# Optimization experiments

Measured on AMD Instinct MI355X. Metric: run time of the kernel, lower is better.

Reference implementation:

```python
import jax, jax.numpy as jnp
import numpy as np
import math

D_MODEL = 1024
N_HEADS = 16
D_HEAD = D_MODEL // N_HEADS
DECAY_MAX = 0.99  # buggy torch init: only the LAST head's decay rate survives the loop
LN_EPS = 1e-5


def setup_inputs() -> dict:
    key = jax.random.key(0)
    ks = jax.random.split(key, 12)
    B, S = 2, 2048
    x = jax.random.normal(ks[0], (B, S, D_MODEL), dtype=jnp.float32)
    def w(k):
        return jax.random.normal(k, (D_MODEL, D_MODEL), dtype=jnp.float32) * 0.02
    return {
        "x": x,
        "Wq": w(ks[1]), "bq": jnp.zeros((D_MODEL,), jnp.float32),
        "Wk": w(ks[2]), "bk": jnp.zeros((D_MODEL,), jnp.float32),
        "Wv": w(ks[3]), "bv": jnp.zeros((D_MODEL,), jnp.float32),
        "Wg": w(ks[4]), "bg": jnp.zeros((D_MODEL,), jnp.float32),
        "Wo": w(ks[5]), "bo": jnp.zeros((D_MODEL,), jnp.float32),
        "gamma": jnp.ones((D_MODEL,), jnp.float32),
        "beta": jnp.zeros((D_MODEL,), jnp.float32),
    }


def _decay_mask(S):
    # faithful to torch buffer: decay_matrix[i,j] = DECAY_MAX**(i-j) for j<=i else 0
    i = jnp.arange(S, dtype=jnp.float32)[:, None]
    j = jnp.arange(S, dtype=jnp.float32)[None, :]
    diff = i - j
    return jnp.where(diff >= 0, jnp.power(jnp.float32(DECAY_MAX), diff), 0.0)  # [S,S]


def reference(x, Wq, bq, Wk, bk, Wv, bv, Wg, bg, Wo, bo, gamma, beta):
    B, S, D = x.shape
    H, DH = N_HEADS, D_HEAD
    # projections -> [B,H,S,DH]
    Q = (x @ Wq + bq).reshape(B, S, H, DH).transpose(0, 2, 1, 3)
    K = (x @ Wk + bk).reshape(B, S, H, DH).transpose(0, 2, 1, 3)
    V = (x @ Wv + bv).reshape(B, S, H, DH).transpose(0, 2, 1, 3)
    scores = jnp.einsum('bhsd,bhtd->bhst', Q, K) / math.sqrt(DH)  # [B,H,S,S]
    mask = _decay_mask(S)  # [S,S], broadcast over B,H (head-independent per torch bug)
    retained = jnp.einsum('bhst,bhtd->bhsd', scores * mask, V)
    retained = retained.transpose(0, 2, 1, 3).reshape(B, S, D)
    # LayerNorm over last dim
    mu = jnp.mean(retained, axis=-1, keepdims=True)
    var = jnp.var(retained, axis=-1, keepdims=True)
    normed = (retained - mu) * jax.lax.rsqrt(var + LN_EPS) * gamma + beta
    G = jax.nn.sigmoid(x @ Wg + bg)
    return (normed * G) @ Wo + bo  # dropout = identity (eval)
```

## Files before the change

kernel.cpp:

```cpp
#include <hip/hip_runtime.h>

typedef __attribute__((ext_vector_type(4))) float f32x4;
typedef __attribute__((ext_vector_type(8))) short bf16x8;
typedef unsigned short USHORT;

static __device__ __forceinline__ float bf2f(USHORT u) {
    return __uint_as_float(((unsigned)u) << 16);
}
static __device__ __forceinline__ USHORT f2bf(float f) {
    unsigned u = __float_as_uint(f);
    unsigned r = u + 0x7FFF + ((u >> 16) & 1);
    return (USHORT)(r >> 16);
}

#define GLDS16(gp, lp) __builtin_amdgcn_global_load_lds(                      \
    (const __attribute__((address_space(1))) unsigned int*)(gp),              \
    (__attribute__((address_space(3))) unsigned int*)(lp), 16, 0, 0)

#define FULL_BARRIER() asm volatile("s_waitcnt vmcnt(0) lgkmcnt(0)\ns_barrier" ::: "memory")

#define D64 0.52559648f
#define L2D (-0.014499569695115089f)

struct PrepArgs { const float* src[5]; USHORT* dst[5]; const float* x; USHORT* xb; };

__global__ __launch_bounds__(256) void k_prep(PrepArgs pa) {
    const int z = blockIdx.z;
    const int tid = threadIdx.x;
    __shared__ USHORT t[64][65];
    if (z < 5) {
        const float* __restrict__ W  = pa.src[z];
        USHORT* __restrict__      WT = pa.dst[z];
        const int k0 = blockIdx.y * 64, n0 = blockIdx.x * 64;
#pragma unroll
        for (int s = 0; s < 4; s++) {
            int slot = tid + s * 256;
            int row = slot >> 4, c4 = (slot & 15) * 4;
            float4 vv = *(const float4*)&W[(size_t)(k0 + row) * 1024 + n0 + c4];
            t[row][c4 + 0] = f2bf(vv.x);
            t[row][c4 + 1] = f2bf(vv.y);
            t[row][c4 + 2] = f2bf(vv.z);
            t[row][c4 + 3] = f2bf(vv.w);
        }
        __syncthreads();
#pragma unroll
        for (int s = 0; s < 2; s++) {
            int slot = tid + s * 256;
            int n = slot >> 3, c8 = (slot & 7) * 8;
            USHORT tmp[8];
#pragma unroll
            for (int u = 0; u < 8; u++) tmp[u] = t[c8 + u][n];
            *(int4*)&WT[(size_t)(n0 + n) * 1024 + k0 + c8] = *(int4*)tmp;
        }
    } else {
        const int bi = blockIdx.y * 16 + blockIdx.x;
        const float* xs = pa.x + (size_t)bi * 16384;
        USHORT* xd = pa.xb + (size_t)bi * 16384;
#pragma unroll
        for (int u = 0; u < 16; u++) {
            int idx = u * 1024 + tid * 4;
            float4 v = *(const float4*)&xs[idx];
            *(ushort4*)&xd[idx] = make_ushort4(f2bf(v.x), f2bf(v.y), f2bf(v.z), f2bf(v.w));
        }
    }
}

struct GArgs {
    const USHORT* A;
    const USHORT* W[4];
    const float*  bias[4];
    void*         dst[4];
    USHORT*       dstv;
    float         scale[4];
    int           mode[4];
};


__global__ __launch_bounds__(256, 2) void k_gemm(GArgs ga) {
    const int z = blockIdx.z;
    const USHORT* __restrict__ A  = ga.A;
    const USHORT* __restrict__ BT = ga.W[z];
    __shared__ USHORT As[2][128 * 32];
    __shared__ USHORT Bs[2][128 * 32];
    const int tid = threadIdx.x;
    const int m0 = blockIdx.y * 128, n0 = blockIdx.x * 128;
    const int w = tid >> 6, l = tid & 63, lr = l & 15, q = l >> 4;
    const int wr = w >> 1, wc = w & 1;
    const int srow = tid >> 2, sco = (tid & 3) * 8;
    const int scol = (((tid & 3) ^ ((tid >> 3) & 3)) << 3);
    const int kread = ((q ^ ((lr >> 1) & 3)) << 3);
    f32x4 acc[4][4] = {};
    GLDS16(&A [(size_t)(m0 + srow)      * 1024 + scol], &As[0][srow * 32 + sco]);
    GLDS16(&A [(size_t)(m0 + srow + 64) * 1024 + scol], &As[0][(srow + 64) * 32 + sco]);
    GLDS16(&BT[(size_t)(n0 + srow)      * 1024 + scol], &Bs[0][srow * 32 + sco]);
    GLDS16(&BT[(size_t)(n0 + srow + 64) * 1024 + scol], &Bs[0][(srow + 64) * 32 + sco]);
    for (int kt = 0; kt < 32; kt++) {
        const int cur = kt & 1;
        FULL_BARRIER();
        if (kt + 1 < 32) {
            const int k1 = (kt + 1) * 32;
            const int nxt = 1 - cur;
            GLDS16(&A [(size_t)(m0 + srow)      * 1024 + k1 + scol], &As[nxt][srow * 32 + sco]);
            GLDS16(&A [(size_t)(m0 + srow + 64) * 1024 + k1 + scol], &As[nxt][(srow + 64) * 32 + sco]);
            GLDS16(&BT[(size_t)(n0 + srow)      * 1024 + k1 + scol], &Bs[nxt][srow * 32 + sco]);
            GLDS16(&BT[(size_t)(n0 + srow + 64) * 1024 + k1 + scol], &Bs[nxt][(srow + 64) * 32 + sco]);
        }
        bf16x8 af[4], bfr[4];
#pragma unroll
        for (int mi = 0; mi < 4; mi++)
            af[mi] = *(const bf16x8*)&As[cur][(wr * 64 + mi * 16 + lr) * 32 + kread];
#pragma unroll
        for (int ni = 0; ni < 4; ni++)
            bfr[ni] = *(const bf16x8*)&Bs[cur][(wc * 64 + ni * 16 + lr) * 32 + kread];
#pragma unroll
        for (int mi = 0; mi < 4; mi++)
#pragma unroll
            for (int ni = 0; ni < 4; ni++)
                acc[mi][ni] = __builtin_amdgcn_mfma_f32_16x16x32_bf16(
                    af[mi], bfr[ni], acc[mi][ni], 0, 0, 0);
    }
    const float scale = ga.scale[z];
    const int mode = ga.mode[z];
    const float* __restrict__ bias = ga.bias[z];
#pragma unroll
    for (int ni = 0; ni < 4; ni++) {
        int col = n0 + wc * 64 + ni * 16 + lr;
        float bv = bias[col];
#pragma unroll
        for (int mi = 0; mi < 4; mi++) {
            int r0 = m0 + wr * 64 + mi * 16 + q * 4;
            float vr[4];
#pragma unroll
            for (int r = 0; r < 4; r++) {
                float v = acc[mi][ni][r] + bv;
                if (mode == 1) v = 1.0f / (1.0f + __expf(-v));
                vr[r] = v * scale;
            }
            if (mode == 3) {
                float* df = (float*)ga.dst[z];
#pragma unroll
                for (int r = 0; r < 4; r++)
                    df[(size_t)(r0 + r) * 1024 + col] = vr[r];
            } else if (mode == 2) {
                int b = r0 >> 11, s = r0 & 2047;
                int h = col >> 6, d = col & 63;
                const float NP1 = 1.0101010101010102f;
                float c0 = exp2f(-L2D * (float)(s & 63));
                float c1 = c0 * NP1, c2 = c1 * NP1, c3 = c2 * NP1;
                *(ushort4*)&ga.dstv[(size_t)(((b * 16 + h) * 64) + d) * 2048 + s] =
                    make_ushort4(f2bf(vr[0] * c0), f2bf(vr[1] * c1),
                                 f2bf(vr[2] * c2), f2bf(vr[3] * c3));
            } else {
                USHORT* db = (USHORT*)ga.dst[z];
#pragma unroll
                for (int r = 0; r < 4; r++)
                    db[(size_t)(r0 + r) * 1024 + col] = f2bf(vr[r]);
            }
        }
    }
}

__global__ __launch_bounds__(256, 2) void k_gemm_out(const USHORT* __restrict__ A,
                                                     const USHORT* __restrict__ BT,
                                                     const float* __restrict__ bias,
                                                     float* __restrict__ C) {
    __shared__ USHORT As[2][64 * 32];
    __shared__ USHORT Bs[2][128 * 32];
    const int tid = threadIdx.x;
    const int m0 = blockIdx.y * 64, n0 = blockIdx.x * 128;
    const int w = tid >> 6, l = tid & 63, lr = l & 15, q = l >> 4;
    const int srow = tid >> 2, sco = (tid & 3) * 8;
    const int scol = (((tid & 3) ^ ((tid >> 3) & 3)) << 3);
    const int kread = ((q ^ ((lr >> 1) & 3)) << 3);
    f32x4 acc[4][2] = {};
    GLDS16(&A [(size_t)(m0 + srow)      * 1024 + scol], &As[0][srow * 32 + sco]);
    GLDS16(&BT[(size_t)(n0 + srow)      * 1024 + scol], &Bs[0][srow * 32 + sco]);
    GLDS16(&BT[(size_t)(n0 + srow + 64) * 1024 + scol], &Bs[0][(srow + 64) * 32 + sco]);
    for (int kt = 0; kt < 32; kt++) {
        const int cur = kt & 1;
        FULL_BARRIER();
        if (kt + 1 < 32) {
            const int k1 = (kt + 1) * 32;
            const int nxt = 1 - cur;
            GLDS16(&A [(size_t)(m0 + srow)      * 1024 + k1 + scol], &As[nxt][srow * 32 + sco]);
            GLDS16(&BT[(size_t)(n0 + srow)      * 1024 + k1 + scol], &Bs[nxt][srow * 32 + sco]);
            GLDS16(&BT[(size_t)(n0 + srow + 64) * 1024 + k1 + scol], &Bs[nxt][(srow + 64) * 32 + sco]);
        }
        bf16x8 af[4], bfr[2];
#pragma unroll
        for (int mi = 0; mi < 4; mi++)
            af[mi] = *(const bf16x8*)&As[cur][(mi * 16 + lr) * 32 + kread];
#pragma unroll
        for (int ni = 0; ni < 2; ni++)
            bfr[ni] = *(const bf16x8*)&Bs[cur][(w * 32 + ni * 16 + lr) * 32 + kread];
#pragma unroll
        for (int mi = 0; mi < 4; mi++)
#pragma unroll
            for (int ni = 0; ni < 2; ni++)
                acc[mi][ni] = __builtin_amdgcn_mfma_f32_16x16x32_bf16(
                    af[mi], bfr[ni], acc[mi][ni], 0, 0, 0);
    }
#pragma unroll
    for (int ni = 0; ni < 2; ni++) {
        const int col = n0 + w * 32 + ni * 16 + lr;
        const float bv = bias[col];
#pragma unroll
        for (int mi = 0; mi < 4; mi++) {
            const int r0 = m0 + mi * 16 + q * 4;
#pragma unroll
            for (int r = 0; r < 4; r++)
                C[(size_t)(r0 + r) * 1024 + col] = acc[mi][ni][r] + bv;
        }
    }
}

#define LDSA(buf, kh) (((buf) * 2 + (kh)) * 8192)
#define LDSB(buf, kh) (32768 + ((buf) * 2 + (kh)) * 8192)
#define BAR() asm volatile("s_barrier" ::: "memory")
#define VM8() asm volatile("s_waitcnt vmcnt(8)" ::: "memory")

#define STAGE_A(ks, kh, buf) do {                                             \
    const USHORT* s_ = aBase + (ks) * 64 + (kh) * 32;                         \
    GLDS16(s_,          &lds[LDSA(buf, kh) + ldsT]);                          \
    GLDS16(s_ + 131072, &lds[LDSA(buf, kh) + 4096 + ldsT]); } while (0)

#define STAGE_B(ks, kh, buf) do {                                             \
    const USHORT* s_ = bBase + (ks) * 64 + (kh) * 32;                         \
    GLDS16(s_,          &lds[LDSB(buf, kh) + ldsT]);                          \
    GLDS16(s_ + 131072, &lds[LDSB(buf, kh) + 4096 + ldsT]); } while (0)

#define PHASE256(buf, kh, mg, LOADB, STAGE_STMT, WAITSTMT) do {               \
    _Pragma("unroll")                                                         \
    for (int mi = 0; mi < 4; mi++)                                            \
        af[mi] = *(const bf16x8*)&lds[LDSA(buf, kh) + aoff + ((mg) * 4 + mi) * 512]; \
    if (LOADB) {                                                              \
        _Pragma("unroll")                                                     \
        for (int ni = 0; ni < 4; ni++)                                        \
            bfrag[ni] = *(const bf16x8*)&lds[LDSB(buf, kh) + boff + ni * 512];\
    }                                                                         \
    STAGE_STMT;                                                               \
    BAR();                                                                    \
    __builtin_amdgcn_s_setprio(1);                                            \
    _Pragma("unroll")                                                         \
    for (int mi = 0; mi < 4; mi++)                                            \
        _Pragma("unroll")                                                     \
        for (int ni = 0; ni < 4; ni++)                                        \
            acc[(mg) * 4 + mi][ni] = __builtin_amdgcn_mfma_f32_16x16x32_bf16( \
                af[mi], bfrag[ni], acc[(mg) * 4 + mi][ni], 0, 0, 0);          \
    __builtin_amdgcn_s_setprio(0);                                            \
    WAITSTMT;                                                                 \
    BAR();                                                                    \
} while (0)

__global__ __launch_bounds__(512, 2) void k_gemm256(GArgs ga) {
    extern __shared__ USHORT lds[];
    int bid = blockIdx.x + 4 * (blockIdx.y + 16 * blockIdx.z);
    bid = (bid & 7) * 32 + (bid >> 3);
    const int bz = bid >> 6;
    const int by = (bid >> 2) & 15;
    const int bx = bid & 3;
    const int z = bz;
    const USHORT* __restrict__ A  = ga.A;
    const USHORT* __restrict__ BT = ga.W[z];
    const int m0 = by * 256, n0 = bx * 256;
    const int tid = threadIdx.x;
    const int wid = tid >> 6, l = tid & 63, lr = l & 15, q = l >> 4;
    const int wr = wid >> 2, wc = wid & 3;
    const int srow = tid >> 2;
    const int scol = (((tid & 3) ^ ((tid >> 3) & 3)) << 3);
    const USHORT* aBase = A  + (size_t)(m0 + srow) * 1024 + scol;
    const USHORT* bBase = BT + (size_t)(n0 + srow) * 1024 + scol;
    const int ldsT = tid * 8;
    const int kread = ((q ^ ((lr >> 1) & 3)) << 3);
    const int aoff = (wr * 128 + lr) * 32 + kread;
    const int boff = (wc * 64 + lr) * 32 + kread;
    f32x4 acc[8][4] = {};
    bf16x8 af[4], bfrag[4];

    STAGE_A(0, 0, 0); STAGE_B(0, 0, 0);
    STAGE_A(0, 1, 0); STAGE_B(0, 1, 0);
    STAGE_A(1, 0, 1); STAGE_B(1, 0, 1);
    VM8();
    BAR();

    for (int kt = 0; kt < 16; kt += 2) {
        const int ks1 = kt + 1;
        const int ks2 = (kt + 2 < 16) ? kt + 2 : 15;
        const int ks3 = (kt + 2 < 16) ? kt + 2 : 15;
        const int ks4 = (kt + 3 < 16) ? kt + 3 : 15;
        PHASE256(0, 0, 0, 1, STAGE_A(ks1, 1, 1), (void)0);
        PHASE256(0, 0, 1, 0, STAGE_B(ks1, 1, 1), VM8());
        PHASE256(0, 1, 0, 1, STAGE_A(ks2, 0, 0), (void)0);
        PHASE256(0, 1, 1, 0, STAGE_B(ks2, 0, 0), VM8());
        PHASE256(1, 0, 0, 1, STAGE_A(ks3, 1, 0), (void)0);
        PHASE256(1, 0, 1, 0, STAGE_B(ks3, 1, 0), VM8());
        PHASE256(1, 1, 0, 1, STAGE_A(ks4, 0, 1), (void)0);
        PHASE256(1, 1, 1, 0, STAGE_B(ks4, 0, 1), VM8());
    }

    const float scale = ga.scale[z];
    const int mode = ga.mode[z];
    const float* __restrict__ bias = ga.bias[z];
#pragma unroll
    for (int ni = 0; ni < 4; ni++) {
        int col = n0 + wc * 64 + ni * 16 + lr;
        float bv = bias[col];
#pragma unroll
        for (int mi = 0; mi < 8; mi++) {
            int r0 = m0 + wr * 128 + mi * 16 + q * 4;
            float vr[4];
#pragma unroll
            for (int r = 0; r < 4; r++) {
                float v = acc[mi][ni][r] + bv;
                if (mode == 1) v = 1.0f / (1.0f + __expf(-v));
                vr[r] = v * scale;
            }
            if (mode == 3) {
                float* df = (float*)ga.dst[z];
#pragma unroll
                for (int r = 0; r < 4; r++)
                    df[(size_t)(r0 + r) * 1024 + col] = vr[r];
            } else if (mode == 2) {
                int b = r0 >> 11, s = r0 & 2047;
                int h = col >> 6, d = col & 63;
                const float NP1 = 1.0101010101010102f;
                float c0 = exp2f(-L2D * (float)(s & 63));
                float c1 = c0 * NP1, c2 = c1 * NP1, c3 = c2 * NP1;
                *(ushort4*)&ga.dstv[(size_t)(((b * 16 + h) * 64) + d) * 2048 + s] =
                    make_ushort4(f2bf(vr[0] * c0), f2bf(vr[1] * c1),
                                 f2bf(vr[2] * c2), f2bf(vr[3] * c3));
            } else {
                USHORT* db = (USHORT*)ga.dst[z];
#pragma unroll
                for (int r = 0; r < 4; r++)
                    db[(size_t)(r0 + r) * 1024 + col] = f2bf(vr[r]);
            }
        }
    }
}

__global__ __launch_bounds__(256) void k_attn_u(const USHORT* __restrict__ K,
                                                const USHORT* __restrict__ VT,
                                                float* __restrict__ U) {
    const int bh = blockIdx.x, c = blockIdx.y;
    const int b = bh >> 4, h = bh & 15;
    const int tid = threadIdx.x, w = tid >> 6, l = tid & 63, lr = l & 15, q = l >> 4;
    __shared__ USHORT KT[64 * 72];
    __shared__ USHORT Vs[64 * 72];
#pragma unroll
    for (int s = 0; s < 2; s++) {
        int slot = tid + s * 256;
        int row = slot >> 3, co = (slot & 7) * 8;
        USHORT kv[8];
        *(int4*)kv = *(const int4*)&K[(size_t)(b * 2048 + c * 64 + row) * 1024 + h * 64 + co];
#pragma unroll
        for (int u = 0; u < 8; u++) KT[(co + u) * 72 + row] = kv[u];
        *(int4*)&Vs[row * 72 + co] =
            *(const int4*)&VT[(size_t)(bh * 64 + row) * 2048 + c * 64 + co];
    }
    __syncthreads();
    f32x4 acc[4] = {};
    bf16x8 av[2];
#pragma unroll
    for (int kk = 0; kk < 2; kk++)
        av[kk] = *(const bf16x8*)&Vs[(w * 16 + lr) * 72 + kk * 32 + q * 8];
#pragma unroll
    for (int dkt = 0; dkt < 4; dkt++)
#pragma unroll
        for (int kk = 0; kk < 2; kk++) {
            bf16x8 bk = *(const bf16x8*)&KT[(dkt * 16 + lr) * 72 + kk * 32 + q * 8];
            acc[dkt] = __builtin_amdgcn_mfma_f32_16x16x32_bf16(av[kk], bk, acc[dkt], 0, 0, 0);
        }
    float* slot = U + (size_t)(bh * 32 + c) * 4096;
#pragma unroll
    for (int dkt = 0; dkt < 4; dkt++)
#pragma unroll
        for (int r = 0; r < 4; r++)
            slot[(w * 16 + q * 4 + r) * 64 + dkt * 16 + lr] = acc[dkt][r] * D64;
}

__global__ __launch_bounds__(256) void k_scan(float* __restrict__ U) {
    const int bh = blockIdx.x;
    const int idx4 = blockIdx.y * 256 + threadIdx.x;
    float* base = U + (size_t)bh * 32 * 4096 + idx4 * 4;
    float4 s = make_float4(0.f, 0.f, 0.f, 0.f);
    for (int c = 0; c < 32; c++) {
        float* p = base + (size_t)c * 4096;
        float4 v = *(const float4*)p;
        s.x = s.x * D64 + v.x;
        s.y = s.y * D64 + v.y;
        s.z = s.z * D64 + v.z;
        s.w = s.w * D64 + v.w;
        *(float4*)p = s;
    }
}

__global__ __launch_bounds__(256, 2) void k_apply(const USHORT* __restrict__ Q,
                                                  const USHORT* __restrict__ K,
                                                  const USHORT* __restrict__ VT,
                                                  const float* __restrict__ U,
                                                  USHORT* __restrict__ R,
                                                  float* __restrict__ stats) {
    const int bh = blockIdx.x, c = blockIdx.y;
    const int b = bh >> 4, h = bh & 15;
    const int i0 = c * 64;
    const int tid = threadIdx.x, w = tid >> 6, l = tid & 63, lr = l & 15, q = l >> 4;
    __shared__ USHORT Qs[64 * 72];
    __shared__ USHORT Ks[64 * 72];
    __shared__ USHORT Vs[64 * 72];
    __shared__ USHORT Ps[4][16 * 72];
    __shared__ unsigned Spk[4096];
#pragma unroll
    for (int s = 0; s < 2; s++) {
        int slot = tid + s * 256;
        int row = slot >> 3, c8 = (slot & 7) * 8;
        USHORT q8[8];
        *(int4*)q8 = *(const int4*)&Q[(size_t)(b * 2048 + i0 + row) * 1024 + h * 64 + c8];
        const float fr = exp2f(L2D * (float)row);
#pragma unroll
        for (int u = 0; u < 8; u++) q8[u] = f2bf(bf2f(q8[u]) * fr);
        *(int4*)&Qs[row * 72 + c8] = *(int4*)q8;
        *(int4*)&Ks[row * 72 + c8] =
            *(const int4*)&K[(size_t)(b * 2048 + i0 + row) * 1024 + h * 64 + c8];
        *(int4*)&Vs[row * 72 + c8] =
            *(const int4*)&VT[(size_t)(bh * 64 + row) * 2048 + i0 + c8];
    }
    if (c > 0) {
        const float* p = U + (size_t)(bh * 32 + (c - 1)) * 4096 + tid * 16;
        float sa[16];
#pragma unroll
        for (int u4 = 0; u4 < 4; u4++) {
            float4 uv = *(const float4*)(p + u4 * 4);
            sa[u4 * 4 + 0] = uv.x; sa[u4 * 4 + 1] = uv.y;
            sa[u4 * 4 + 2] = uv.z; sa[u4 * 4 + 3] = uv.w;
        }
#pragma unroll
        for (int u = 0; u < 16; u++) {
            USHORT hi = f2bf(sa[u]);
            float  lo = sa[u] - bf2f(hi);
            Spk[tid * 16 + u] = (unsigned)hi | ((unsigned)f2bf(lo) << 16);
        }
    }
    __syncthreads();
    bf16x8 bqf[2];
#pragma unroll
    for (int kk = 0; kk < 2; kk++)
        bqf[kk] = *(const bf16x8*)&Qs[(w * 16 + lr) * 72 + kk * 32 + q * 8];
    f32x4 accr[4] = {};
    if (c > 0) {
#pragma unroll
        for (int dt = 0; dt < 4; dt++)
#pragma unroll
            for (int kk = 0; kk < 2; kk++) {
                const unsigned* sp = &Spk[(dt * 16 + lr) * 64 + kk * 32 + q * 8];
                uint4 pa = *(const uint4*)sp;
                uint4 pb = *(const uint4*)(sp + 4);
                unsigned pk[8] = { pa.x, pa.y, pa.z, pa.w, pb.x, pb.y, pb.z, pb.w };
                bf16x8 hi, lo;
#pragma unroll
                for (int u = 0; u < 8; u++) {
                    hi[u] = (short)(pk[u] & 0xffffu);
                    lo[u] = (short)(pk[u] >> 16);
                }
                accr[dt] = __builtin_amdgcn_mfma_f32_16x16x32_bf16(hi, bqf[kk], accr[dt], 0, 0, 0);
                accr[dt] = __builtin_amdgcn_mfma_f32_16x16x32_bf16(lo, bqf[kk], accr[dt], 0, 0, 0);
            }
    }
    {
        f32x4 accp[4] = {};
#pragma unroll
        for (int kk = 0; kk < 2; kk++)
#pragma unroll
            for (int jt = 0; jt < 4; jt++) {
                bf16x8 akf = *(const bf16x8*)&Ks[(jt * 16 + lr) * 72 + kk * 32 + q * 8];
                accp[jt] = __builtin_amdgcn_mfma_f32_16x16x32_bf16(akf, bqf[kk], accp[jt], 0, 0, 0);
            }
        const int ii = w * 16 + lr;
#pragma unroll
        for (int jt = 0; jt < 4; jt++) {
            const int jj = jt * 16 + q * 4;
            float v0 = (jj + 0 <= ii) ? accp[jt][0] : 0.0f;
            float v1 = (jj + 1 <= ii) ? accp[jt][1] : 0.0f;
            float v2 = (jj + 2 <= ii) ? accp[jt][2] : 0.0f;
            float v3 = (jj + 3 <= ii) ? accp[jt][3] : 0.0f;
            unsigned w0 = __builtin_amdgcn_perm(
                __float_as_uint(v1), __float_as_uint(v0), 0x07060302u);
            unsigned w1 = __builtin_amdgcn_perm(
                __float_as_uint(v3), __float_as_uint(v2), 0x07060302u);
            *(uint2*)&Ps[w][lr * 72 + jt * 16 + q * 4] = make_uint2(w0, w1);
        }
        asm volatile("s_waitcnt lgkmcnt(0)" ::: "memory");
#pragma unroll
        for (int kk = 0; kk < 2; kk++) {
            bf16x8 bpf = *(const bf16x8*)&Ps[w][lr * 72 + kk * 32 + q * 8];
#pragma unroll
            for (int dt = 0; dt < 4; dt++) {
                bf16x8 avf = *(const bf16x8*)&Vs[(dt * 16 + lr) * 72 + kk * 32 + q * 8];
                accr[dt] = __builtin_amdgcn_mfma_f32_16x16x32_bf16(avf, bpf, accr[dt], 0, 0, 0);
            }
        }
    }
    {
        float s1 = 0.f, s2 = 0.f;
#pragma unroll
        for (int dt = 0; dt < 4; dt++)
#pragma unroll
            for (int r = 0; r < 4; r++) {
                float v = accr[dt][r];
                s1 += v; s2 += v * v;
            }
        s1 += __shfl_down(s1, 32); s2 += __shfl_down(s2, 32);
        s1 += __shfl_down(s1, 16); s2 += __shfl_down(s2, 16);
        if (q == 0) {
            int row = b * 2048 + i0 + w * 16 + lr;
            *(float2*)&stats[((size_t)row * 16 + h) * 2] = make_float2(s1, s2);
        }
    }
    {
        const int i = i0 + w * 16 + lr;
#pragma unroll
        for (int dt = 0; dt < 4; dt++) {
            f32x4 a = accr[dt];
            *(ushort4*)&R[(size_t)(b * 2048 + i) * 1024 + h * 64 + dt * 16 + q * 4] =
                make_ushort4(f2bf(a[0]), f2bf(a[1]), f2bf(a[2]), f2bf(a[3]));
        }
    }
}

__global__ __launch_bounds__(256) void k_ln_gate(const USHORT* __restrict__ R,
                                                 const USHORT* __restrict__ G,
                                                 const float* __restrict__ stats,
                                                 const float* __restrict__ gamma,
                                                 const float* __restrict__ beta,
                                                 USHORT* __restrict__ NG) {
    const int row = blockIdx.x, tid = threadIdx.x;
    float s1 = 0.f, s2 = 0.f;
    const float* sp = &stats[(size_t)row * 32];
#pragma unroll
    for (int hh = 0; hh < 8; hh++) {
        float4 v = *(const float4*)(sp + hh * 4);
        s1 += v.x + v.z; s2 += v.y + v.w;
    }
    const float mu  = s1 * (1.0f / 1024.0f);
    const float var = s2 * (1.0f / 1024.0f) - mu * mu;
    const float inv = rsqrtf(fmaxf(var, 0.0f) + 1e-5f);
    ushort4 rv = *(const ushort4*)&R[(size_t)row * 1024 + tid * 4];
    ushort4 g4 = *(const ushort4*)&G[(size_t)row * 1024 + tid * 4];
    float4 gm = *(const float4*)&gamma[tid * 4];
    float4 bt = *(const float4*)&beta[tid * 4];
    float  vv[4]  = { bf2f(rv.x), bf2f(rv.y), bf2f(rv.z), bf2f(rv.w) };
    USHORT gg[4]  = { g4.x, g4.y, g4.z, g4.w };
    float  gmm[4] = { gm.x, gm.y, gm.z, gm.w };
    float  btt[4] = { bt.x, bt.y, bt.z, bt.w };
    USHORT o4[4];
#pragma unroll
    for (int u = 0; u < 4; u++) {
        float nv = (vv[u] - mu) * inv * gmm[u] + btt[u];
        o4[u] = f2bf(nv * bf2f(gg[u]));
    }
    *(ushort4*)&NG[(size_t)row * 1024 + tid * 4] = make_ushort4(o4[0], o4[1], o4[2], o4[3]);
}

extern "C" void kernel_launch(void* const* d_in, const int* in_sizes, int n_in,
                              void* d_out, int out_size, void* d_ws, size_t ws_size,
                              hipStream_t stream) {
    const float* x     = (const float*)d_in[0];
    const float* Wq    = (const float*)d_in[1];
    const float* bq    = (const float*)d_in[2];
    const float* Wk    = (const float*)d_in[3];
    const float* bk    = (const float*)d_in[4];
    const float* Wv    = (const float*)d_in[5];
    const float* bv    = (const float*)d_in[6];
    const float* Wg    = (const float*)d_in[7];
    const float* bg    = (const float*)d_in[8];
    const float* Wo    = (const float*)d_in[9];
    const float* bo    = (const float*)d_in[10];
    const float* gamma = (const float*)d_in[11];
    const float* beta  = (const float*)d_in[12];

    char* ws = (char*)d_ws;
    const size_t MB = 1 << 20;
    USHORT* WqT = (USHORT*)(ws + 0 * MB);
    USHORT* WkT = (USHORT*)(ws + 2 * MB);
    USHORT* WvT = (USHORT*)(ws + 4 * MB);
    USHORT* WgT = (USHORT*)(ws + 6 * MB);
    USHORT* WoT = (USHORT*)(ws + 8 * MB);
    USHORT* Qb  = (USHORT*)(ws + 10 * MB);
    USHORT* Kb  = (USHORT*)(ws + 18 * MB);
    USHORT* VTb = (USHORT*)(ws + 26 * MB);
    USHORT* Gb  = (USHORT*)(ws + 34 * MB);
    float*  Sts = (float*) (ws + 42 * MB);
    USHORT* NGb = Qb;
    USHORT* Xb  = (USHORT*)d_out;
    float*  Ust = (float*)d_out;

    {
        PrepArgs pa;
        pa.src[0] = Wq; pa.src[1] = Wk; pa.src[2] = Wv; pa.src[3] = Wg; pa.src[4] = Wo;
        pa.dst[0] = WqT; pa.dst[1] = WkT; pa.dst[2] = WvT; pa.dst[3] = WgT; pa.dst[4] = WoT;
        pa.x = x; pa.xb = Xb;
        k_prep<<<dim3(16, 16, 6), 256, 0, stream>>>(pa);
    }
    {
        static int s_256ok = -1;
        if (s_256ok < 0) {
            hipError_t e = hipFuncSetAttribute(
                reinterpret_cast<const void*>(&k_gemm256),
                hipFuncAttributeMaxDynamicSharedMemorySize, 131072);
            s_256ok = (e == hipSuccess) ? 1 : 0;
        }
        GArgs ga;
        ga.A = Xb;
        ga.W[0] = WqT; ga.W[1] = WkT; ga.W[2] = WvT; ga.W[3] = WgT;
        ga.bias[0] = bq; ga.bias[1] = bk; ga.bias[2] = bv; ga.bias[3] = bg;
        ga.dst[0] = Qb; ga.dst[1] = Kb; ga.dst[2] = nullptr; ga.dst[3] = Gb;
        ga.dstv = VTb;
        ga.scale[0] = 0.125f; ga.scale[1] = 1.0f; ga.scale[2] = 1.0f; ga.scale[3] = 1.0f;
        ga.mode[0] = 0; ga.mode[1] = 0; ga.mode[2] = 2; ga.mode[3] = 1;
        if (s_256ok)
            k_gemm256<<<dim3(4, 16, 4), 512, 131072, stream>>>(ga);
        else
            k_gemm<<<dim3(8, 32, 4), 256, 0, stream>>>(ga);
    }
    k_attn_u<<<dim3(32, 32), 256, 0, stream>>>(Kb, VTb, Ust);
    k_scan<<<dim3(32, 4), 256, 0, stream>>>(Ust);
    k_apply<<<dim3(32, 32), 256, 0, stream>>>(Qb, Kb, VTb, Ust, Kb, Sts);
    k_ln_gate<<<4096, 256, 0, stream>>>(Kb, Gb, Sts, gamma, beta, NGb);
    k_gemm_out<<<dim3(8, 64), 256, 0, stream>>>(NGb, WoT, bo, (float*)d_out);
}
```

Measured before the change: 210.7 us.

## Fuse LayerNorm and gating into output GEMM A-tile staging, pad scan LDS

Removes the k_ln_gate kernel. A small k_ln_stats kernel now computes per-row mean and inverse std, and k_gemm_out normalizes and gates R*G while staging each A tile into LDS. The intent is to avoid writing and re-reading the NG intermediate and to drop a kernel launch. The cost is that the LN and gate math runs 8 times per row (once per N-block) with register loads instead of async global_load_lds, which may hurt GEMM overlap. It also pads the Spk LDS stride in k_apply to 68 to reduce bank conflicts, and splits k_scan into more, smaller blocks for parallelism.

```diff
diff --git a/kernel.cpp b/kernel.cpp
--- a/kernel.cpp
+++ b/kernel.cpp
@@ -160,7 +160,50 @@
     }
 }
 
-__global__ __launch_bounds__(256, 2) void k_gemm_out(const USHORT* __restrict__ A,
+__global__ __launch_bounds__(256) void k_ln_stats(const float* __restrict__ stats,
+                                                  float* __restrict__ muinv) {
+    const int row = blockIdx.x * 256 + threadIdx.x;
+    const float* sp = &stats[(size_t)row * 32];
+    float s1 = 0.f, s2 = 0.f;
+#pragma unroll
+    for (int hh = 0; hh < 8; hh++) {
+        float4 v = *(const float4*)(sp + hh * 4);
+        s1 += v.x + v.z; s2 += v.y + v.w;
+    }
+    const float mu  = s1 * (1.0f / 1024.0f);
+    const float var = s2 * (1.0f / 1024.0f) - mu * mu;
+    const float inv = rsqrtf(fmaxf(var, 0.0f) + 1e-5f);
+    *(float2*)&muinv[(size_t)row * 2] = make_float2(mu, inv);
+}
+
+#define STAGE_NG(KC, BUF) do {                                                \
+    const int cb_ = (KC) + scol;                                              \
+    int4 rv4_ = *(const int4*)&R[(size_t)arow * 1024 + cb_];                  \
+    int4 gv4_ = *(const int4*)&G[(size_t)arow * 1024 + cb_];                  \
+    float4 gmA_ = *(const float4*)&gamma[cb_];                                \
+    float4 gmB_ = *(const float4*)&gamma[cb_ + 4];                            \
+    float4 btA_ = *(const float4*)&beta[cb_];                                 \
+    float4 btB_ = *(const float4*)&beta[cb_ + 4];                             \
+    USHORT rr_[8]; *(int4*)rr_ = rv4_;                                        \
+    USHORT gg_[8]; *(int4*)gg_ = gv4_;                                        \
+    float gmv_[8] = { gmA_.x, gmA_.y, gmA_.z, gmA_.w,                         \
+                      gmB_.x, gmB_.y, gmB_.z, gmB_.w };                       \
+    float btv_[8] = { btA_.x, btA_.y, btA_.z, btA_.w,                         \
+                      btB_.x, btB_.y, btB_.z, btB_.w };                       \
+    USHORT o_[8];                                                             \
+    _Pragma("unroll")                                                         \
+    for (int u = 0; u < 8; u++) {                                             \
+        float nv = (bf2f(rr_[u]) - mu) * inv * gmv_[u] + btv_[u];             \
+        o_[u] = f2bf(nv * bf2f(gg_[u]));                                      \
+    }                                                                         \
+    *(int4*)&As[BUF][srow * 32 + sco] = *(int4*)o_;                           \
+} while (0)
+
+__global__ __launch_bounds__(256, 2) void k_gemm_out(const USHORT* __restrict__ R,
+                                                     const USHORT* __restrict__ G,
+                                                     const float* __restrict__ muinv,
+                                                     const float* __restrict__ gamma,
+                                                     const float* __restrict__ beta,
                                                      const USHORT* __restrict__ BT,
                                                      const float* __restrict__ bias,
                                                      float* __restrict__ C) {
@@ -172,17 +215,19 @@
     const int srow = tid >> 2, sco = (tid & 3) * 8;
     const int scol = (((tid & 3) ^ ((tid >> 3) & 3)) << 3);
     const int kread = ((q ^ ((lr >> 1) & 3)) << 3);
+    const int arow = m0 + srow;
+    const float2 mi2 = *(const float2*)&muinv[(size_t)arow * 2];
+    const float mu = mi2.x, inv = mi2.y;
     f32x4 acc[4][2] = {};
-    GLDS16(&A [(size_t)(m0 + srow)      * 1024 + scol], &As[0][srow * 32 + sco]);
+    STAGE_NG(0, 0);
     GLDS16(&BT[(size_t)(n0 + srow)      * 1024 + scol], &Bs[0][srow * 32 + sco]);
     GLDS16(&BT[(size_t)(n0 + srow + 64) * 1024 + scol], &Bs[0][(srow + 64) * 32 + sco]);
     for (int kt = 0; kt < 32; kt++) {
         const int cur = kt & 1;
         FULL_BARRIER();
+        const int k1 = (kt + 1) * 32;
+        const int nxt = 1 - cur;
         if (kt + 1 < 32) {
-            const int k1 = (kt + 1) * 32;
-            const int nxt = 1 - cur;
-            GLDS16(&A [(size_t)(m0 + srow)      * 1024 + k1 + scol], &As[nxt][srow * 32 + sco]);
             GLDS16(&BT[(size_t)(n0 + srow)      * 1024 + k1 + scol], &Bs[nxt][srow * 32 + sco]);
             GLDS16(&BT[(size_t)(n0 + srow + 64) * 1024 + k1 + scol], &Bs[nxt][(srow + 64) * 32 + sco]);
         }
@@ -199,6 +244,8 @@
             for (int ni = 0; ni < 2; ni++)
                 acc[mi][ni] = __builtin_amdgcn_mfma_f32_16x16x32_bf16(
                     af[mi], bfr[ni], acc[mi][ni], 0, 0, 0);
+        if (kt + 1 < 32)
+            STAGE_NG(k1, nxt);
     }
 #pragma unroll
     for (int ni = 0; ni < 2; ni++) {
@@ -379,9 +426,9 @@
             slot[(w * 16 + q * 4 + r) * 64 + dkt * 16 + lr] = acc[dkt][r] * D64;
 }
 
-__global__ __launch_bounds__(256) void k_scan(float* __restrict__ U) {
+__global__ __launch_bounds__(128) void k_scan(float* __restrict__ U) {
     const int bh = blockIdx.x;
-    const int idx4 = blockIdx.y * 256 + threadIdx.x;
+    const int idx4 = blockIdx.y * 128 + threadIdx.x;
     float* base = U + (size_t)bh * 32 * 4096 + idx4 * 4;
     float4 s = make_float4(0.f, 0.f, 0.f, 0.f);
     for (int c = 0; c < 32; c++) {
@@ -409,7 +456,7 @@
     __shared__ USHORT Ks[64 * 72];
     __shared__ USHORT Vs[64 * 72];
     __shared__ USHORT Ps[4][16 * 72];
-    __shared__ unsigned Spk[4096];
+    __shared__ unsigned Spk[64 * 68];
 #pragma unroll
     for (int s = 0; s < 2; s++) {
         int slot = tid + s * 256;
@@ -434,11 +481,12 @@
             sa[u4 * 4 + 0] = uv.x; sa[u4 * 4 + 1] = uv.y;
             sa[u4 * 4 + 2] = uv.z; sa[u4 * 4 + 3] = uv.w;
         }
+        const int srw = tid >> 2, sq = tid & 3;
 #pragma unroll
         for (int u = 0; u < 16; u++) {
             USHORT hi = f2bf(sa[u]);
             float  lo = sa[u] - bf2f(hi);
-            Spk[tid * 16 + u] = (unsigned)hi | ((unsigned)f2bf(lo) << 16);
+            Spk[srw * 68 + sq * 16 + u] = (unsigned)hi | ((unsigned)f2bf(lo) << 16);
         }
     }
     __syncthreads();
@@ -452,7 +500,7 @@
         for (int dt = 0; dt < 4; dt++)
 #pragma unroll
             for (int kk = 0; kk < 2; kk++) {
-                const unsigned* sp = &Spk[(dt * 16 + lr) * 64 + kk * 32 + q * 8];
+                const unsigned* sp = &Spk[(dt * 16 + lr) * 68 + kk * 32 + q * 8];
                 uint4 pa = *(const uint4*)sp;
                 uint4 pb = *(const uint4*)(sp + 4);
                 unsigned pk[8] = { pa.x, pa.y, pa.z, pa.w, pb.x, pb.y, pb.z, pb.w };
@@ -525,40 +573,6 @@
                 make_ushort4(f2bf(a[0]), f2bf(a[1]), f2bf(a[2]), f2bf(a[3]));
         }
     }
-}
-
-__global__ __launch_bounds__(256) void k_ln_gate(const USHORT* __restrict__ R,
-                                                 const USHORT* __restrict__ G,
-                                                 const float* __restrict__ stats,
-                                                 const float* __restrict__ gamma,
-                                                 const float* __restrict__ beta,
-                                                 USHORT* __restrict__ NG) {
-    const int row = blockIdx.x, tid = threadIdx.x;
-    float s1 = 0.f, s2 = 0.f;
-    const float* sp = &stats[(size_t)row * 32];
-#pragma unroll
-    for (int hh = 0; hh < 8; hh++) {
-        float4 v = *(const float4*)(sp + hh * 4);
-        s1 += v.x + v.z; s2 += v.y + v.w;
-    }
-    const float mu  = s1 * (1.0f / 1024.0f);
-    const float var = s2 * (1.0f / 1024.0f) - mu * mu;
-    const float inv = rsqrtf(fmaxf(var, 0.0f) + 1e-5f);
-    ushort4 rv = *(const ushort4*)&R[(size_t)row * 1024 + tid * 4];
-    ushort4 g4 = *(const ushort4*)&G[(size_t)row * 1024 + tid * 4];
-    float4 gm = *(const float4*)&gamma[tid * 4];
-    float4 bt = *(const float4*)&beta[tid * 4];
-    float  vv[4]  = { bf2f(rv.x), bf2f(rv.y), bf2f(rv.z), bf2f(rv.w) };
-    USHORT gg[4]  = { g4.x, g4.y, g4.z, g4.w };
-    float  gmm[4] = { gm.x, gm.y, gm.z, gm.w };
-    float  btt[4] = { bt.x, bt.y, bt.z, bt.w };
-    USHORT o4[4];
-#pragma unroll
-    for (int u = 0; u < 4; u++) {
-        float nv = (vv[u] - mu) * inv * gmm[u] + btt[u];
-        o4[u] = f2bf(nv * bf2f(gg[u]));
-    }
-    *(ushort4*)&NG[(size_t)row * 1024 + tid * 4] = make_ushort4(o4[0], o4[1], o4[2], o4[3]);
 }
 
 extern "C" void kernel_launch(void* const* d_in, const int* in_sizes, int n_in,
@@ -590,7 +604,7 @@
     USHORT* VTb = (USHORT*)(ws + 26 * MB);
     USHORT* Gb  = (USHORT*)(ws + 34 * MB);
     float*  Sts = (float*) (ws + 42 * MB);
-    USHORT* NGb = Qb;
+    float*  MuI = (float*) (ws + 10 * MB);
     USHORT* Xb  = (USHORT*)d_out;
     float*  Ust = (float*)d_out;
 
@@ -623,8 +637,9 @@
             k_gemm<<<dim3(8, 32, 4), 256, 0, stream>>>(ga);
     }
     k_attn_u<<<dim3(32, 32), 256, 0, stream>>>(Kb, VTb, Ust);
-    k_scan<<<dim3(32, 4), 256, 0, stream>>>(Ust);
+    k_scan<<<dim3(32, 8), 128, 0, stream>>>(Ust);
     k_apply<<<dim3(32, 32), 256, 0, stream>>>(Qb, Kb, VTb, Ust, Kb, Sts);
-    k_ln_gate<<<4096, 256, 0, stream>>>(Kb, Gb, Sts, gamma, beta, NGb);
-    k_gemm_out<<<dim3(8, 64), 256, 0, stream>>>(NGb, WoT, bo, (float*)d_out);
-}
+    k_ln_stats<<<16, 256, 0, stream>>>(Sts, MuI);
+    k_gemm_out<<<dim3(8, 64), 256, 0, stream>>>(Kb, Gb, MuI, gamma, beta, WoT, bo,
+                                                (float*)d_out);
+}
```

Measured after the change: 220.2 us. +4.5%, slower.
